# Kernel optimization log

Hardware: AMD Instinct MI355X
Metric: run time of the kernel (lower is better)

Reference implementation:

```python
import jax, jax.numpy as jnp
import numpy as np

N_NODES = 50000
N_EDGES = 800000
IN, HID, OUT = 256, 128, 64


def setup_inputs() -> dict:
    key = jax.random.key(0)
    ks = jax.random.split(key, 5)
    return {
        "x": jax.random.normal(ks[0], (N_NODES, IN), dtype=jnp.float32),
        "W1": jax.random.normal(ks[1], (IN, HID), dtype=jnp.float32) / np.sqrt(IN),
        "b1": jnp.zeros((HID,), dtype=jnp.float32),
        "W2": jax.random.normal(ks[2], (HID, OUT), dtype=jnp.float32) / np.sqrt(HID),
        "b2": jnp.zeros((OUT,), dtype=jnp.float32),
        "src": jax.random.randint(ks[3], (N_EDGES,), 0, N_NODES, dtype=jnp.int32),
        "dst": jax.random.randint(ks[4], (N_EDGES,), 0, N_NODES, dtype=jnp.int32),
    }


def _graph_conv(h, W, b, src, dst, norm_src, norm_dst, n_nodes):
    # DGL GraphConv, norm='both': y = D_dst^{-1/2} A D_src^{-1/2} h W + b
    # Project first (smaller feature dim for the SpMM), linearity makes it exact.
    h = h @ W                                     # [N, d_out]
    msg = (h * norm_src[:, None])[src]            # gather per-edge   [E, d_out]
    agg = jax.ops.segment_sum(msg, dst, num_segments=n_nodes)  # [N, d_out]
    return agg * norm_dst[:, None] + b


def reference(x, W1, b1, W2, b2, src, dst):
    n = x.shape[0]
    ones = jnp.ones(src.shape[0], dtype=jnp.float32)
    out_deg = jnp.zeros(n, jnp.float32).at[src].add(ones)
    in_deg = jnp.zeros(n, jnp.float32).at[dst].add(ones)
    norm_src = jax.lax.rsqrt(jnp.maximum(out_deg, 1.0))
    norm_dst = jax.lax.rsqrt(jnp.maximum(in_deg, 1.0))

    h = _graph_conv(x, W1, b1, src, dst, norm_src, norm_dst, n)
    h = jax.nn.relu(h)
    return _graph_conv(h, W2, b2, src, dst, norm_src, norm_dst, n)
```

## Files before the change

### kernel.cpp

```cpp
#include <hip/hip_runtime.h>

#define NN 50000
#define NE 800000
#define NPAD 50176
#define NSLICE 32
#define ESL 25000
#define HPN 25088
#define HPW 12544
#define FPN 12544
#define GB2 196
#define FB 128
#define NB 196

typedef __attribute__((ext_vector_type(8))) short bf16x8;
typedef __attribute__((ext_vector_type(4))) float f32x4;

__device__ __forceinline__ float u2f(unsigned u) { return __uint_as_float(u); }
__device__ __forceinline__ unsigned f2u(float f) { return __float_as_uint(f); }
__device__ __forceinline__ unsigned short f2bf(float f) {
    unsigned u = f2u(f);
    return (unsigned short)((u + (((u >> 16) & 1u) + 0x7fffu)) >> 16);
}
__device__ __forceinline__ void acc8(float* ax, uint4 u) {
    ax[0] += u2f(u.x << 16); ax[1] += u2f(u.x & 0xffff0000u);
    ax[2] += u2f(u.y << 16); ax[3] += u2f(u.y & 0xffff0000u);
    ax[4] += u2f(u.z << 16); ax[5] += u2f(u.z & 0xffff0000u);
    ax[6] += u2f(u.w << 16); ax[7] += u2f(u.w & 0xffff0000u);
}

__global__ __launch_bounds__(1024) void hist_wtrans_kernel(
    const int* __restrict__ src, const int* __restrict__ dst,
    unsigned* __restrict__ cnt_sl,
    const float* __restrict__ W1, const float* __restrict__ W2,
    unsigned short* __restrict__ Wh1, unsigned short* __restrict__ Wl1,
    unsigned short* __restrict__ Wh2, unsigned short* __restrict__ Wl2,
    int* __restrict__ done_cnt) {
    if (blockIdx.x == 0 && threadIdx.x == 0) *done_cnt = 0;
    const int b = blockIdx.x;
    if (b >= 128) {
        float w;
        unsigned short *ph, *pl;
        int f;
        if (b < 160) {
            int i = (b - 128) * 1024 + threadIdx.x;
            int k = i >> 7, n = i & 127;
            f = (((n >> 4) * 32 + (k >> 3)) * 16 + (n & 15)) * 8 + (k & 7);
            w = W1[i]; ph = Wh1; pl = Wl1;
        } else {
            int i = (b - 160) * 1024 + threadIdx.x;
            int k = i >> 6, n = i & 63;
            f = (((n >> 4) * 16 + (k >> 3)) * 16 + (n & 15)) * 8 + (k & 7);
            w = W2[i]; ph = Wh2; pl = Wl2;
        }
        unsigned u = f2u(w);
        float lo = w - u2f(u & 0xffff0000u);
        ph[f] = (unsigned short)(u >> 16);
        pl[f] = (unsigned short)(f2u(lo) >> 16);
        return;
    }
    __shared__ unsigned lcnt[HPW];
    const int side = b & 1;
    const int slice = (b >> 1) & (NSLICE - 1);
    const int part = b >> 6;
    const int* __restrict__ arr = side ? dst : src;
    const int base = part * HPN;
    for (int j = threadIdx.x; j < HPW; j += 1024) lcnt[j] = 0;
    __syncthreads();
    const int e0 = slice * ESL;
    for (int i = e0 + threadIdx.x; i < e0 + ESL; i += 1024) {
        int v = arr[i] - base;
        if ((unsigned)v < (unsigned)HPN)
            atomicAdd(&lcnt[v >> 1], 1u << ((v & 1) * 16));
    }
    __syncthreads();
    unsigned* o = cnt_sl + (size_t)b * HPW;
    for (int j = threadIdx.x; j < HPW; j += 1024) o[j] = lcnt[j];
}

__global__ __launch_bounds__(256) void norm_scanAB_kernel(
    const unsigned* __restrict__ cnt_sl, float* __restrict__ ns,
    float* __restrict__ nd, int* __restrict__ presum,
    int* __restrict__ pref, int* __restrict__ blk_sum,
    int* __restrict__ blk_ofs, int* __restrict__ done_cnt, int n) {
    __shared__ int lds[256];
    __shared__ int is_last;
    int i = blockIdx.x * 256 + threadIdx.x;
    int d_total = 0;
    if (i < n) {
        int part = (i >= HPN) ? 1 : 0;
        int w = (i - part * HPN) >> 1;
        int sh = (i & 1) * 16;
        int s_total = 0;
#pragma unroll
        for (int sl = 0; sl < NSLICE; sl++) {
            int bb = part * 64 + sl * 2;
            s_total += (cnt_sl[(size_t)bb * HPW + w] >> sh) & 0xffff;
            int c = (cnt_sl[(size_t)(bb + 1) * HPW + w] >> sh) & 0xffff;
            presum[sl * NPAD + i] = d_total;
            d_total += c;
        }
        ns[i] = rsqrtf(fmaxf((float)s_total, 1.0f));
        nd[i] = rsqrtf(fmaxf((float)d_total, 1.0f));
    }
    lds[threadIdx.x] = d_total;
    __syncthreads();
    for (int ofs = 1; ofs < 256; ofs <<= 1) {
        int t = (threadIdx.x >= ofs) ? lds[threadIdx.x - ofs] : 0;
        __syncthreads();
        lds[threadIdx.x] += t;
        __syncthreads();
    }
    if (i < n) pref[i] = lds[threadIdx.x] - d_total;
    if (threadIdx.x == 255) blk_sum[blockIdx.x] = lds[255];
    __threadfence();
    if (threadIdx.x == 0) {
        int c = atomicAdd(done_cnt, 1);
        is_last = (c == gridDim.x - 1);
    }
    __syncthreads();
    if (!is_last) return;
    __threadfence();
    int v = (threadIdx.x < gridDim.x) ? blk_sum[threadIdx.x] : 0;
    __syncthreads();
    lds[threadIdx.x] = v;
    __syncthreads();
    for (int ofs = 1; ofs < 256; ofs <<= 1) {
        int t = (threadIdx.x >= ofs) ? lds[threadIdx.x - ofs] : 0;
        __syncthreads();
        lds[threadIdx.x] += t;
        __syncthreads();
    }
    if (threadIdx.x < gridDim.x) blk_ofs[threadIdx.x] = lds[threadIdx.x] - v;
}

__global__ __launch_bounds__(1024) void gemm1_fill_kernel(
    const float* __restrict__ A, const unsigned short* __restrict__ Wh,
    const unsigned short* __restrict__ Wl, const float* __restrict__ norm_src,
    unsigned short* __restrict__ out,
    const int* __restrict__ src, const int* __restrict__ dst,
    const int* __restrict__ pref, const int* __restrict__ blk_ofs,
    const int* __restrict__ presum, int* __restrict__ eidx, int M) {
    __shared__ int cur[FPN];
    const int b = blockIdx.x;
    if (b < GB2) {
        constexpr int N = 128, K = 256;
        constexpr int NT = N / 16, KC = K / 32;
        const int wave = threadIdx.x >> 6;
        const int lane = threadIdx.x & 63;
        const int ln = lane & 15;
        const int qk = lane >> 4;
        const int m0 = b * 256 + wave * 16;
        const int mA = m0 + ln;
        const float* Arow = A + (size_t)(mA < M ? mA : (M - 1)) * K + qk * 8;
        const bf16x8* BH = (const bf16x8*)Wh;
        const bf16x8* BL = (const bf16x8*)Wl;

        f32x4 acc[NT];
#pragma unroll
        for (int t = 0; t < NT; t++) acc[t] = (f32x4){0.f, 0.f, 0.f, 0.f};

        float4 a0 = *(const float4*)(Arow);
        float4 a1 = *(const float4*)(Arow + 4);
#pragma unroll
        for (int c = 0; c < KC; ++c) {
            float4 n0, n1;
            if (c + 1 < KC) {
                n0 = *(const float4*)(Arow + (c + 1) * 32);
                n1 = *(const float4*)(Arow + (c + 1) * 32 + 4);
            }
            float av[8] = {a0.x, a0.y, a0.z, a0.w, a1.x, a1.y, a1.z, a1.w};
            bf16x8 ah, al;
#pragma unroll
            for (int j = 0; j < 8; ++j) {
                unsigned u = f2u(av[j]);
                float lo = av[j] - u2f(u & 0xffff0000u);
                ah[j] = (short)(u >> 16);
                al[j] = (short)(f2u(lo) >> 16);
            }
            const int fb = c * 4 + qk;
#pragma unroll
            for (int t = 0; t < NT; ++t) {
                bf16x8 bh = BH[(t * (K / 8) + fb) * 16 + ln];
                bf16x8 bl = BL[(t * (K / 8) + fb) * 16 + ln];
                acc[t] = __builtin_amdgcn_mfma_f32_16x16x32_bf16(ah, bh, acc[t], 0, 0, 0);
                acc[t] = __builtin_amdgcn_mfma_f32_16x16x32_bf16(ah, bl, acc[t], 0, 0, 0);
                acc[t] = __builtin_amdgcn_mfma_f32_16x16x32_bf16(al, bh, acc[t], 0, 0, 0);
            }
            a0 = n0; a1 = n1;
        }
        float sc[4];
#pragma unroll
        for (int r = 0; r < 4; ++r) {
            int row = m0 + qk * 4 + r;
            sc[r] = (row < M) ? norm_src[row] : 0.f;
        }
#pragma unroll
        for (int t = 0; t < NT; ++t)
#pragma unroll
            for (int r = 0; r < 4; ++r) {
                int row = m0 + qk * 4 + r;
                if (row < M) out[(size_t)row * N + t * 16 + ln] = f2bf(acc[t][r] * sc[r]);
            }
        return;
    }
    const int fb = b - GB2;
    const int slice = fb >> 2;
    const int part = fb & 3;
    const int base = part * FPN;
    for (int j = threadIdx.x; j < FPN; j += 1024) {
        int gi = base + j;
        cur[j] = (gi < NN) ? pref[gi] + blk_ofs[gi >> 8] + presum[slice * NPAD + gi] : 0;
    }
    __syncthreads();
    const int e0 = slice * ESL;
    for (int i = e0 + threadIdx.x; i < e0 + ESL; i += 1024) {
        int v = dst[i] - base;
        if ((unsigned)v < (unsigned)FPN) {
            int pos = atomicAdd(&cur[v], 1);
            eidx[pos] = src[i];
        }
    }
}

__global__ __launch_bounds__(256) void layer2_kernel(
    const unsigned* __restrict__ hs1, const int* __restrict__ eidx,
    const int* __restrict__ pref, const int* __restrict__ blk_ofs,
    const float* __restrict__ norm_src, const float* __restrict__ norm_dst,
    const float* __restrict__ bias, const unsigned short* __restrict__ Wh,
    const unsigned short* __restrict__ Wl, unsigned short* __restrict__ hs2, int n) {
    __shared__ unsigned lh1[16 * 68];
    const int wave = threadIdx.x >> 6;
    const int lane = threadIdx.x & 63;
    const int nb = blockIdx.x * 16;
    const int q = lane >> 4;
    const int p = lane & 15;

    for (int j = 0; j < 4; ++j) {
        const int node = nb + wave * 4 + j;
        float ax[8];
#pragma unroll
        for (int k = 0; k < 8; ++k) ax[k] = 0.f;
        unsigned pk[4] = {0u, 0u, 0u, 0u};
        if (node < n) {
            int beg = pref[node] + blk_ofs[node >> 8];
            int end = (node + 1 < n) ? pref[node + 1] + blk_ofs[(node + 1) >> 8] : NE;
            int e = beg;
            for (; e + 15 < end; e += 16) {
                int i0 = eidx[e + q];
                int i1 = eidx[e + 4 + q];
                int i2 = eidx[e + 8 + q];
                int i3 = eidx[e + 12 + q];
                uint4 u0 = *(const uint4*)(hs1 + (size_t)i0 * 64 + p * 4);
                uint4 u1 = *(const uint4*)(hs1 + (size_t)i1 * 64 + p * 4);
                uint4 u2 = *(const uint4*)(hs1 + (size_t)i2 * 64 + p * 4);
                uint4 u3 = *(const uint4*)(hs1 + (size_t)i3 * 64 + p * 4);
                acc8(ax, u0);
                acc8(ax, u1);
                acc8(ax, u2);
                acc8(ax, u3);
            }
            for (; e + 7 < end; e += 8) {
                int i0 = eidx[e + q];
                int i1 = eidx[e + 4 + q];
                uint4 u0 = *(const uint4*)(hs1 + (size_t)i0 * 64 + p * 4);
                uint4 u1 = *(const uint4*)(hs1 + (size_t)i1 * 64 + p * 4);
                acc8(ax, u0);
                acc8(ax, u1);
            }
            for (; e < end; e += 4) {
                int ee = e + q;
                bool ok = ee < end;
                int i0 = eidx[ok ? ee : beg];
                uint4 u0 = *(const uint4*)(hs1 + (size_t)i0 * 64 + p * 4);
                if (ok) acc8(ax, u0);
            }
#pragma unroll
            for (int k = 0; k < 8; ++k) {
                ax[k] += __shfl_xor(ax[k], 16);
                ax[k] += __shfl_xor(ax[k], 32);
            }
            float sc = norm_dst[node];
            float4 b0 = *(const float4*)(bias + p * 8);
            float4 b1 = *(const float4*)(bias + p * 8 + 4);
            float bb[8] = {b0.x, b0.y, b0.z, b0.w, b1.x, b1.y, b1.z, b1.w};
#pragma unroll
            for (int k = 0; k < 4; ++k) {
                float rlo = fmaxf(ax[2 * k] * sc + bb[2 * k], 0.f);
                float rhi = fmaxf(ax[2 * k + 1] * sc + bb[2 * k + 1], 0.f);
                pk[k] = (unsigned)f2bf(rlo) | ((unsigned)f2bf(rhi) << 16);
            }
        }
        if (q == 0)
            *(uint4*)&lh1[(wave * 4 + j) * 68 + p * 4] = *(uint4*)pk;
    }
    __syncthreads();

    const int ln = lane & 15;
    const int qk = lane >> 4;
    const int t = wave;
    const bf16x8* BH = (const bf16x8*)Wh;
    const bf16x8* BL = (const bf16x8*)Wl;
    f32x4 acc = (f32x4){0.f, 0.f, 0.f, 0.f};
#pragma unroll
    for (int c = 0; c < 4; ++c) {
        bf16x8 ah = *(const bf16x8*)&lh1[ln * 68 + c * 16 + qk * 4];
        const int fb = c * 4 + qk;
        bf16x8 bh = BH[(t * 16 + fb) * 16 + ln];
        bf16x8 bl = BL[(t * 16 + fb) * 16 + ln];
        acc = __builtin_amdgcn_mfma_f32_16x16x32_bf16(ah, bh, acc, 0, 0, 0);
        acc = __builtin_amdgcn_mfma_f32_16x16x32_bf16(ah, bl, acc, 0, 0, 0);
    }
#pragma unroll
    for (int r = 0; r < 4; ++r) {
        int node = nb + qk * 4 + r;
        if (node < n)
            hs2[(size_t)node * 64 + t * 16 + ln] = f2bf(acc[r] * norm_src[node]);
    }
}

__global__ __launch_bounds__(256) void gather64_kernel(
    const unsigned* __restrict__ hs, const int* __restrict__ eidx,
    const int* __restrict__ pref, const int* __restrict__ blk_ofs,
    const float* __restrict__ norm_dst, const float* __restrict__ bias,
    float* __restrict__ out, int n) {
    int wave = (blockIdx.x * blockDim.x + threadIdx.x) >> 6;
    int lane = threadIdx.x & 63;
    if (wave >= n) return;
    int beg = pref[wave] + blk_ofs[wave >> 8];
    int end = (wave + 1 < n) ? pref[wave + 1] + blk_ofs[(wave + 1) >> 8] : NE;
    const int o = lane >> 3;
    const int p = lane & 7;
    float ax[8];
#pragma unroll
    for (int k = 0; k < 8; ++k) ax[k] = 0.f;
    int e = beg;
    for (; e + 15 < end; e += 16) {
        int i0 = eidx[e + o];
        int i1 = eidx[e + 8 + o];
        uint4 u0 = *(const uint4*)(hs + (size_t)i0 * 32 + p * 4);
        uint4 u1 = *(const uint4*)(hs + (size_t)i1 * 32 + p * 4);
        acc8(ax, u0);
        acc8(ax, u1);
    }
    for (; e < end; e += 8) {
        int ee = e + o;
        bool ok = ee < end;
        int i0 = eidx[ok ? ee : beg];
        uint4 u0 = *(const uint4*)(hs + (size_t)i0 * 32 + p * 4);
        if (ok) acc8(ax, u0);
    }
#pragma unroll
    for (int k = 0; k < 8; ++k) {
        ax[k] += __shfl_xor(ax[k], 8);
        ax[k] += __shfl_xor(ax[k], 16);
        ax[k] += __shfl_xor(ax[k], 32);
    }
    if (o == 0) {
        float sc = norm_dst[wave];
        float4 b0 = *(const float4*)(bias + p * 8);
        float4 b1 = *(const float4*)(bias + p * 8 + 4);
        float4 r0, r1;
        r0.x = ax[0] * sc + b0.x;
        r0.y = ax[1] * sc + b0.y;
        r0.z = ax[2] * sc + b0.z;
        r0.w = ax[3] * sc + b0.w;
        r1.x = ax[4] * sc + b1.x;
        r1.y = ax[5] * sc + b1.y;
        r1.z = ax[6] * sc + b1.z;
        r1.w = ax[7] * sc + b1.w;
        *(float4*)(out + (size_t)wave * 64 + p * 8) = r0;
        *(float4*)(out + (size_t)wave * 64 + p * 8 + 4) = r1;
    }
}

extern "C" void kernel_launch(void* const* d_in, const int* in_sizes, int n_in,
                              void* d_out, int out_size, void* d_ws, size_t ws_size,
                              hipStream_t stream) {
    const float* x  = (const float*)d_in[0];
    const float* W1 = (const float*)d_in[1];
    const float* b1 = (const float*)d_in[2];
    const float* W2 = (const float*)d_in[3];
    const float* b2 = (const float*)d_in[4];
    const int* src  = (const int*)d_in[5];
    const int* dst  = (const int*)d_in[6];
    float* out = (float*)d_out;
    char* ws = (char*)d_ws;

    float* norm_src = (float*)(ws);
    float* norm_dst = (float*)(ws + 4 * 50176);
    int*   pref     = (int*)(ws + 4 * 100352);
    int*   blk_sum  = (int*)(ws + 4 * 150528);
    int*   blk_ofs  = (int*)(ws + 4 * 150784);
    int*   done_cnt = (int*)(ws + 4 * 151040);
    int*   eidx     = (int*)(ws + 4 * 151296);
    unsigned short* Wh1 = (unsigned short*)(ws + 4 * 951296);
    unsigned short* Wl1 = (unsigned short*)(ws + 4 * 967680);
    unsigned short* Wh2 = (unsigned short*)(ws + 4 * 984064);
    unsigned short* Wl2 = (unsigned short*)(ws + 4 * 988160);
    unsigned short* hs1 = (unsigned short*)(ws + 4 * 992256);
    unsigned short* hs2 = (unsigned short*)(ws + 4 * 4192256);
    unsigned* cnt_sl    = (unsigned*)(ws + 4 * 5792256);
    int* presum         = (int*)(ws + 4 * 7397888);

    hist_wtrans_kernel<<<168, 1024, 0, stream>>>(src, dst, cnt_sl, W1, W2,
                                                 Wh1, Wl1, Wh2, Wl2, done_cnt);

    norm_scanAB_kernel<<<NB, 256, 0, stream>>>(cnt_sl, norm_src, norm_dst,
                                               presum, pref, blk_sum, blk_ofs,
                                               done_cnt, NN);

    gemm1_fill_kernel<<<GB2 + FB, 1024, 0, stream>>>(
        x, Wh1, Wl1, norm_src, hs1, src, dst, pref, blk_ofs, presum, eidx, NN);

    layer2_kernel<<<3125, 256, 0, stream>>>(
        (const unsigned*)hs1, eidx, pref, blk_ofs, norm_src, norm_dst, b1,
        Wh2, Wl2, hs2, NN);

    gather64_kernel<<<12500, 256, 0, stream>>>(
        (const unsigned*)hs2, eidx, pref, blk_ofs, norm_dst, b2, out, NN);
}
```

Measured before the change: 224.9 us.

## Stage GEMM1 A tiles through swizzled double-buffered LDS via global_load_lds

```diff
diff --git a/kernel.cpp b/kernel.cpp
--- a/kernel.cpp
+++ b/kernel.cpp
@@ -27,6 +27,10 @@
     ax[4] += u2f(u.z << 16); ax[5] += u2f(u.z & 0xffff0000u);
     ax[6] += u2f(u.w << 16); ax[7] += u2f(u.w & 0xffff0000u);
 }
+#define GLOAD_LDS16(GP, LP)                                              \
+    __builtin_amdgcn_global_load_lds(                                    \
+        (const __attribute__((address_space(1))) unsigned*)(GP),         \
+        (__attribute__((address_space(3))) unsigned*)(LP), 16, 0, 0)
 
 __global__ __launch_bounds__(1024) void hist_wtrans_kernel(
     const int* __restrict__ src, const int* __restrict__ dst,
@@ -140,7 +144,7 @@
     const int* __restrict__ src, const int* __restrict__ dst,
     const int* __restrict__ pref, const int* __restrict__ blk_ofs,
     const int* __restrict__ presum, int* __restrict__ eidx, int M) {
-    __shared__ int cur[FPN];
+    __shared__ __align__(16) char shmem[65536];
     const int b = blockIdx.x;
     if (b < GB2) {
         constexpr int N = 128, K = 256;
@@ -150,24 +154,41 @@
         const int ln = lane & 15;
         const int qk = lane >> 4;
         const int m0 = b * 256 + wave * 16;
-        const int mA = m0 + ln;
-        const float* Arow = A + (size_t)(mA < M ? mA : (M - 1)) * K + qk * 8;
+        const int m0b = b * 256;
+        float* sh = (float*)shmem;
         const bf16x8* BH = (const bf16x8*)Wh;
         const bf16x8* BL = (const bf16x8*)Wl;
 
+        auto stage = [&](int p, int c) {
+#pragma unroll
+            for (int h = 0; h < 2; ++h) {
+                const int j = threadIdx.x + h * 1024;
+                const int row = j >> 3;
+                const int sp = (j & 7) ^ (row & 7);
+                int grow = m0b + row;
+                if (grow >= M) grow = M - 1;
+                const float* gp = A + (size_t)grow * K + c * 32 + sp * 4;
+                char* lp = (char*)(sh + p * 8192) + (j & ~63) * 16;
+                GLOAD_LDS16(gp, lp);
+            }
+        };
+
+        const int r = wave * 16 + ln;
+        const int offA0 = r * 128 + (((qk * 2) ^ (ln & 7)) * 16);
+        const int offA1 = r * 128 + (((qk * 2 + 1) ^ (ln & 7)) * 16);
+
         f32x4 acc[NT];
 #pragma unroll
         for (int t = 0; t < NT; t++) acc[t] = (f32x4){0.f, 0.f, 0.f, 0.f};
 
-        float4 a0 = *(const float4*)(Arow);
-        float4 a1 = *(const float4*)(Arow + 4);
-#pragma unroll
+        stage(0, 0);
+        __syncthreads();
+#pragma unroll 2
         for (int c = 0; c < KC; ++c) {
-            float4 n0, n1;
-            if (c + 1 < KC) {
-                n0 = *(const float4*)(Arow + (c + 1) * 32);
-                n1 = *(const float4*)(Arow + (c + 1) * 32 + 4);
-            }
+            if (c + 1 < KC) stage((c + 1) & 1, c + 1);
+            const char* bufc = (const char*)sh + (c & 1) * 32768;
+            float4 a0 = *(const float4*)(bufc + offA0);
+            float4 a1 = *(const float4*)(bufc + offA1);
             float av[8] = {a0.x, a0.y, a0.z, a0.w, a1.x, a1.y, a1.z, a1.w};
             bf16x8 ah, al;
 #pragma unroll
@@ -186,23 +207,24 @@
                 acc[t] = __builtin_amdgcn_mfma_f32_16x16x32_bf16(ah, bl, acc[t], 0, 0, 0);
                 acc[t] = __builtin_amdgcn_mfma_f32_16x16x32_bf16(al, bh, acc[t], 0, 0, 0);
             }
-            a0 = n0; a1 = n1;
+            __syncthreads();
         }
         float sc[4];
 #pragma unroll
-        for (int r = 0; r < 4; ++r) {
-            int row = m0 + qk * 4 + r;
-            sc[r] = (row < M) ? norm_src[row] : 0.f;
+        for (int rr = 0; rr < 4; ++rr) {
+            int row = m0 + qk * 4 + rr;
+            sc[rr] = (row < M) ? norm_src[row] : 0.f;
         }
 #pragma unroll
         for (int t = 0; t < NT; ++t)
 #pragma unroll
-            for (int r = 0; r < 4; ++r) {
-                int row = m0 + qk * 4 + r;
-                if (row < M) out[(size_t)row * N + t * 16 + ln] = f2bf(acc[t][r] * sc[r]);
+            for (int rr = 0; rr < 4; ++rr) {
+                int row = m0 + qk * 4 + rr;
+                if (row < M) out[(size_t)row * N + t * 16 + ln] = f2bf(acc[t][rr] * sc[rr]);
             }
         return;
     }
+    int* cur = (int*)shmem;
     const int fb = b - GB2;
     const int slice = fb >> 2;
     const int part = fb & 3;
```

Measured after the change: 222.4 us. About the same (-1.1%).
